# Kernel optimization log

Measured on AMD Instinct MI355X. Metric: run time of the kernel, lower is better.

The kernel has to match this reference:

```python
import math
import jax, jax.numpy as jnp
import numpy as np

NUM_PRE_NMS = 2000
NMS_THR = 0.7
MIN_SIZE = 16.0
LOG_MAX = math.log(1000.0 / 16)  # clamp on dh, dw as in the torch module

B, A, H, W = 8, 3, 200, 304
STRIDE = 4


def _make_anchors():
    # grid anchors, channel-last anchor ordering to match permute(0,2,3,1)
    sizes = np.array([32.0, 64.0, 128.0], dtype=np.float32)  # A sizes
    ys = (np.arange(H, dtype=np.float32) + 0.5) * STRIDE
    xs = (np.arange(W, dtype=np.float32) + 0.5) * STRIDE
    cy, cx = np.meshgrid(ys, xs, indexing="ij")  # [H,W]
    cx = cx[:, :, None]
    cy = cy[:, :, None]
    half = (sizes / 2.0)[None, None, :]  # [1,1,A]
    anc = np.stack([cx - half, cy - half, cx + half, cy + half], axis=-1)  # [H,W,A,4]
    anc = anc.reshape(-1, 4)  # [H*W*A, 4]
    anc = np.broadcast_to(anc[None], (B, anc.shape[0], 4)).copy()
    return jnp.asarray(anc)


def setup_inputs() -> dict:
    key = jax.random.key(0)
    k1, k2 = jax.random.split(key)
    cls_logits = jax.random.normal(k1, (B, A, H, W), dtype=jnp.float32)
    regs = jax.random.normal(k2, (B, 4 * A, H, W), dtype=jnp.float32) * 0.1
    anchors = _make_anchors()
    return {"cls_logits": cls_logits, "regs": regs, "anchors": anchors,
            "image_h": 800, "image_w": 1216}


def _box_iou(boxes):
    # boxes: [K,4] -> iou [K,K]
    x1, y1, x2, y2 = boxes[:, 0], boxes[:, 1], boxes[:, 2], boxes[:, 3]
    area = (x2 - x1) * (y2 - y1)
    ix1 = jnp.maximum(x1[:, None], x1[None, :])
    iy1 = jnp.maximum(y1[:, None], y1[None, :])
    ix2 = jnp.minimum(x2[:, None], x2[None, :])
    iy2 = jnp.minimum(y2[:, None], y2[None, :])
    iw = jnp.clip(ix2 - ix1, 0.0)
    ih = jnp.clip(iy2 - iy1, 0.0)
    inter = iw * ih
    union = area[:, None] + area[None, :] - inter
    return inter / jnp.maximum(union, 1e-6)


def _nms_one(boxes, valid):
    # boxes sorted by descending score; greedy suppression, fixed-size keep mask
    k = boxes.shape[0]
    iou = _box_iou(boxes)
    later = jnp.arange(k)

    def body(i, keep):
        sup = (iou[i] > NMS_THR) & keep[i] & (later > i)
        return keep & ~sup

    return jax.lax.fori_loop(0, k, body, valid)


def reference(cls_logits, regs, anchors, image_h, image_w):
    b = cls_logits.shape[0]
    # scores/regs in channel-last anchor order (matches permute(0,2,3,1))
    scores = jnp.transpose(cls_logits, (0, 2, 3, 1)).reshape(b, -1)       # [B,N]
    deltas = jnp.transpose(regs, (0, 2, 3, 1)).reshape(b, -1, 4)          # [B,N,4]
    n = scores.shape[1]
    k = min(NUM_PRE_NMS, n)

    top_scores, idx = jax.lax.top_k(scores, k)                            # [B,K]
    top_deltas = jnp.take_along_axis(deltas, idx[:, :, None], axis=1)     # [B,K,4]
    top_anchors = jnp.take_along_axis(anchors, idx[:, :, None], axis=1)   # [B,K,4]

    dx, dy = top_deltas[..., 0], top_deltas[..., 1]
    dh = jnp.minimum(top_deltas[..., 2], LOG_MAX)
    dw = jnp.minimum(top_deltas[..., 3], LOG_MAX)
    ah = top_anchors[..., 3] - top_anchors[..., 1]
    aw = top_anchors[..., 2] - top_anchors[..., 0]
    cx = aw / 2
    cy = ah / 2
    px = cx + dx * aw
    py = cy + dy * ah
    ph = jnp.exp(dh) * ah
    pw = jnp.exp(dw) * aw
    boxes = jnp.stack([px - pw / 2, py - ph / 2, px + pw / 2, py + ph / 2], axis=-1)  # [B,K,4]

    # size filter on clamped coords (as in _nms)
    w_img = jnp.float32(image_w)
    h_img = jnp.float32(image_h)
    bw = jnp.clip(boxes[..., 2], 0.0, w_img) - jnp.clip(boxes[..., 0], 0.0, w_img)
    bh = jnp.clip(boxes[..., 3], 0.0, h_img) - jnp.clip(boxes[..., 1], 0.0, h_img)
    valid = (bw >= MIN_SIZE) & (bh >= MIN_SIZE)

    keep = jax.vmap(_nms_one)(boxes, valid)                               # [B,K]
    out_boxes = boxes * keep[..., None].astype(boxes.dtype)
    return out_boxes, top_scores, keep
```

## Files before the change

kernel.cpp:

```cpp
#include <hip/hip_runtime.h>

#define HWSZ 60800
#define NA 3
#define NTOT 182400
#define KSEL 2000
#define CANDCAP 8192
#define NBATCH 8
#define GSPLIT 128
#define LOG_MAX_F 4.135166556742356f

#define OFF_H1    0
#define OFF_CCNT  65536
#define OFF_DONE  65568
#define ZR_BYTES  65600
#define OFF_SEL   65600
#define OFF_BOX   65728
#define OFF_VALID 321728
#define OFF_SUP   385728
#define OFF_CAND  385728
#define OFF_SUPT  4481728

__device__ __forceinline__ unsigned int xform(float f) {
    unsigned int b = __float_as_uint(f);
    return b ^ ((unsigned int)((int)b >> 31) | 0x80000000u);
}

__device__ __forceinline__ void bar_lds() {
    asm volatile("s_waitcnt lgkmcnt(0)" ::: "memory");
    __builtin_amdgcn_s_barrier();
}

__global__ __launch_bounds__(256) void k_hist_scan(const float* __restrict__ cls,
                                                   unsigned int* __restrict__ hist1,
                                                   unsigned int* __restrict__ done,
                                                   uint4* __restrict__ selinfo) {
    int b = blockIdx.y, part = blockIdx.x, tid = threadIdx.x;
    __shared__ unsigned int h[2048];
    for (int i = tid; i < 2048; i += 256) h[i] = 0u;
    __syncthreads();
    const float4* base4 = (const float4*)(cls + (size_t)b * NTOT);
    const int n4 = NTOT / 4;
    int per = (n4 + GSPLIT - 1) / GSPLIT;
    int lo = part * per, hi = lo + per;
    if (hi > n4) hi = n4;
    for (int i = lo + tid; i < hi; i += 256) {
        float4 v = base4[i];
        atomicAdd(&h[xform(v.x) >> 21], 1u);
        atomicAdd(&h[xform(v.y) >> 21], 1u);
        atomicAdd(&h[xform(v.z) >> 21], 1u);
        atomicAdd(&h[xform(v.w) >> 21], 1u);
    }
    __syncthreads();
    unsigned int* gh = hist1 + b * 2048;
    for (int i = tid; i < 2048; i += 256)
        if (h[i]) atomicAdd(&gh[i], h[i]);

    __shared__ unsigned int slast;
    __syncthreads();
    if (tid == 0) {
        __threadfence();
        unsigned int old = __hip_atomic_fetch_add(&done[b], 1u, __ATOMIC_ACQ_REL,
                                                  __HIP_MEMORY_SCOPE_AGENT);
        slast = (old == GSPLIT - 1) ? 1u : 0u;
    }
    __syncthreads();
    if (!slast) return;

    __shared__ unsigned int sa[2048], sb[2048];
    #pragma unroll
    for (int k = 0; k < 8; ++k) {
        int i = tid + k * 256;
        sa[i] = __hip_atomic_load(&gh[i], __ATOMIC_RELAXED, __HIP_MEMORY_SCOPE_AGENT);
    }
    unsigned int* src = sa; unsigned int* dst = sb;
    for (int d = 1; d < 2048; d <<= 1) {
        __syncthreads();
        #pragma unroll
        for (int k = 0; k < 8; ++k) {
            int i = tid + k * 256;
            dst[i] = src[i] + ((i + d < 2048) ? src[i + d] : 0u);
        }
        unsigned int* t = src; src = dst; dst = t;
    }
    __syncthreads();
    #pragma unroll
    for (int k = 0; k < 8; ++k) {
        int i = tid + k * 256;
        unsigned int c = src[i];
        unsigned int cn = (i < 2047) ? src[i + 1] : 0u;
        if (c >= KSEL && cn < KSEL)
            selinfo[b] = make_uint4((unsigned int)i, cn, KSEL - cn, 0u);
    }
}

__global__ __launch_bounds__(256) void k_gather(const float* __restrict__ cls,
                                                const uint4* __restrict__ selinfo,
                                                unsigned long long* __restrict__ cand,
                                                unsigned int* __restrict__ ccnt) {
    int b = blockIdx.y, part = blockIdx.x, tid = threadIdx.x;
    unsigned int bin = selinfo[b].x;
    __shared__ unsigned long long lbuf[1024];
    __shared__ unsigned int lcnt, gbase;
    if (tid == 0) lcnt = 0u;
    __syncthreads();
    const float4* base4 = (const float4*)(cls + (size_t)b * NTOT);
    const int n4 = NTOT / 4;
    int per = (n4 + GSPLIT - 1) / GSPLIT;
    int lo = part * per, hi = lo + per;
    if (hi > n4) hi = n4;
    for (int i = lo + tid; i < hi; i += 256) {
        float4 v = base4[i];
        float vals[4] = {v.x, v.y, v.z, v.w};
        int idx0 = i * 4;
        #pragma unroll
        for (int q = 0; q < 4; ++q) {
            unsigned int u = xform(vals[q]);
            if ((u >> 21) >= bin) {
                int idx = idx0 + q;
                int a = idx / HWSZ;
                int hw = idx - a * HWSZ;
                unsigned int n = (unsigned int)(hw * NA + a);
                unsigned int pos = atomicAdd(&lcnt, 1u);
                if (pos < 1024u)
                    lbuf[pos] = ((unsigned long long)u << 32) | (unsigned long long)(~n);
            }
        }
    }
    __syncthreads();
    if (tid == 0) {
        unsigned int c = lcnt < 1024u ? lcnt : 1024u;
        gbase = atomicAdd(&ccnt[b], c);
    }
    __syncthreads();
    unsigned int c = lcnt < 1024u ? lcnt : 1024u;
    unsigned int gb = gbase;
    for (unsigned int i = tid; i < c; i += 256) {
        unsigned int p = gb + i;
        if (p < CANDCAP) cand[(size_t)b * CANDCAP + p] = lbuf[i];
    }
}

__global__ __launch_bounds__(256) void k_rank_decode(
        const unsigned long long* __restrict__ cand,
        const unsigned int* __restrict__ ccnt,
        const float* __restrict__ regs,
        const float* __restrict__ anchors,
        const int* __restrict__ img_h,
        const int* __restrict__ img_w,
        float* __restrict__ out_scores,
        float4* __restrict__ boxes_ws,
        unsigned int* __restrict__ valid_ws) {
    int b = blockIdx.y;
    int tid = threadIdx.x;
    unsigned int sc = ccnt[b];
    if (sc > CANDCAP) sc = CANDCAP;
    unsigned int kbase = blockIdx.x * 64;
    if (kbase >= sc) return;
    int ki = tid & 63;
    int q = tid >> 6;
    int lane = tid & 63;
    const unsigned long long* sb_ = cand + (size_t)b * CANDCAP;
    unsigned int r = kbase + (unsigned int)ki;
    unsigned long long mykey = (r < sc) ? sb_[r] : 0ULL;

    unsigned int qs = ((sc + 255u) >> 8) << 6;
    unsigned int lo = (unsigned int)q * qs;
    unsigned int hi = lo + qs;
    if (hi > sc) hi = sc;

    unsigned int cnt = 0u;
    for (unsigned int base = lo; base < hi; base += 64) {
        unsigned long long kj = 0ULL;
        if (base + (unsigned int)lane < hi) kj = sb_[base + lane];
        unsigned int klo = (unsigned int)kj;
        unsigned int khi = (unsigned int)(kj >> 32);
        #pragma unroll
        for (int t = 0; t < 64; ++t) {
            unsigned int lo_ = (unsigned int)__builtin_amdgcn_readlane((int)klo, t);
            unsigned int hi_ = (unsigned int)__builtin_amdgcn_readlane((int)khi, t);
            unsigned long long kt = ((unsigned long long)hi_ << 32) | (unsigned long long)lo_;
            cnt += (kt > mykey) ? 1u : 0u;
        }
    }
    __shared__ unsigned int cntsh[4][64];
    cntsh[q][ki] = cnt;
    __syncthreads();
    if (tid >= 64) return;
    unsigned int rank = cntsh[0][ki] + cntsh[1][ki] + cntsh[2][ki] + cntsh[3][ki];
    if (r >= sc || rank >= KSEL) return;

    int hv = img_h[0];
    int wv = img_w[0];
    float himg = (hv > 0 && hv < 100000) ? (float)hv : __int_as_float(hv);
    float wimg = (wv > 0 && wv < 100000) ? (float)wv : __int_as_float(wv);

    unsigned int u = (unsigned int)(mykey >> 32);
    unsigned int n = ~((unsigned int)mykey);
    unsigned int bits = (u & 0x80000000u) ? (u & 0x7FFFFFFFu) : ~u;
    float score = __uint_as_float(bits);
    int a = (int)(n % NA);
    int hw = (int)(n / NA);
    const float* rp = regs + ((size_t)b * (4 * NA) + 4 * a) * HWSZ + hw;
    float dx = rp[0 * HWSZ];
    float dy = rp[1 * HWSZ];
    float dh = rp[2 * HWSZ];
    float dw = rp[3 * HWSZ];
    const float* ap = anchors + ((size_t)b * NTOT + n) * 4;
    float ax1 = ap[0], ay1 = ap[1], ax2 = ap[2], ay2 = ap[3];
    float ahh = ay2 - ay1;
    float aww = ax2 - ax1;
    float cx = aww * 0.5f;
    float cy = ahh * 0.5f;
    float px = cx + dx * aww;
    float py = cy + dy * ahh;
    dh = fminf(dh, LOG_MAX_F);
    dw = fminf(dw, LOG_MAX_F);
    float ph = expf(dh) * ahh;
    float pw = expf(dw) * aww;
    float x1 = px - pw * 0.5f;
    float y1 = py - ph * 0.5f;
    float x2 = px + pw * 0.5f;
    float y2 = py + ph * 0.5f;
    float bwv = fminf(fmaxf(x2, 0.f), wimg) - fminf(fmaxf(x1, 0.f), wimg);
    float bhv = fminf(fmaxf(y2, 0.f), himg) - fminf(fmaxf(y1, 0.f), himg);
    unsigned int valid = (bwv >= 16.f && bhv >= 16.f) ? 1u : 0u;
    size_t o = (size_t)b * KSEL + rank;
    out_scores[o] = score;
    boxes_ws[o] = make_float4(x1, y1, x2, y2);
    valid_ws[o] = valid;
}

__global__ __launch_bounds__(256) void k_supmat(const float4* __restrict__ boxes_ws,
                                                unsigned long long* __restrict__ sup,
                                                unsigned long long* __restrict__ supT) {
    int ct = blockIdx.x;
    int rt = blockIdx.y;
    int b  = blockIdx.z;
    if (ct * 64 + 63 < rt * 256) return;
    int tid = threadIdx.x;
    __shared__ float4 colbox[64];
    int j0 = ct * 64;
    if (tid < 64) {
        int jl = j0 + tid;
        colbox[tid] = (jl < KSEL) ? boxes_ws[(size_t)b * KSEL + jl]
                                  : make_float4(0.f, 0.f, 0.f, 0.f);
    }
    __syncthreads();
    int i = rt * 256 + tid;
    if (i >= KSEL) return;
    float4 bi = boxes_ws[(size_t)b * KSEL + i];
    float area_i = (bi.z - bi.x) * (bi.w - bi.y);
    unsigned long long word = 0ULL;
    #pragma unroll 8
    for (int jj = 0; jj < 64; ++jj) {
        int j = j0 + jj;
        float4 bj = colbox[jj];
        float area_j = (bj.z - bj.x) * (bj.w - bj.y);
        float ix1 = fmaxf(bi.x, bj.x);
        float iy1 = fmaxf(bi.y, bj.y);
        float ix2 = fminf(bi.z, bj.z);
        float iy2 = fminf(bi.w, bj.w);
        float iw = fmaxf(ix2 - ix1, 0.f);
        float ih = fmaxf(iy2 - iy1, 0.f);
        float inter = iw * ih;
        float uni = area_i + area_j - inter;
        float iou = inter / fmaxf(uni, 1e-6f);
        bool s = (j > i) && (j < KSEL) && (iou > 0.7f);
        if (s) word |= (1ULL << jj);
    }
    if (ct >= (i >> 6))
        sup[((size_t)b * KSEL + i) * 32 + ct] = word;

    if (ct == rt * 4 + (tid >> 6)) {
        int lane = tid & 63;
        unsigned long long cm = 0ULL;
        #pragma unroll
        for (int j = 0; j < 64; ++j) {
            unsigned long long t = __ballot((word >> j) & 1ULL);
            if (lane == j) cm = t;
        }
        supT[((size_t)b * 32 + ct) * 64 + lane] = cm;
    }
}

#define LOAD_TILE(wnext, buf)                                                \
    {                                                                        \
        int w_ = (wnext);                                                    \
        _Pragma("unroll")                                                    \
        for (int k = 0; k < 4; ++k) {                                        \
            int lr_ = (tid >> 4) + k * 16;                                   \
            int grow_ = w_ * 64 + lr_;                                       \
            if (grow_ > KSEL - 1) grow_ = KSEL - 1;                          \
            int pp_ = (2 * p + 1 >= w_) ? p : 15;                            \
            buf[k] = srowp[(size_t)grow_ * 16 + pp_];                        \
        }                                                                    \
    }

#define PROCESS_TILE(w, buf)                                                 \
    {                                                                        \
        bar_lds();                                                           \
        int w_ = (w);                                                        \
        unsigned long long pend_ =                                           \
            ((unsigned long long)accw[w_ * 2 + 1] << 32)                     \
            | (unsigned long long)accw[w_ * 2];                              \
        unsigned long long cand_ = kws[w_] & ~pend_;                         \
        unsigned int clo_ = __builtin_amdgcn_readfirstlane((unsigned int)cand_);        \
        unsigned int chi_ = __builtin_amdgcn_readfirstlane((unsigned int)(cand_ >> 32));\
        unsigned long long cur_ = ((unsigned long long)chi_ << 32)           \
                                  | (unsigned long long)clo_;                \
        if (cur_) {                                                          \
            unsigned long long cmw_ = colT[w_ * 64 + lane];                  \
            unsigned long long k_ = cur_;                                    \
            for (;;) {                                                       \
                unsigned long long sup_ = __ballot((k_ & cmw_) != 0ULL);     \
                unsigned long long k2_ = cur_ & ~sup_;                       \
                if (k2_ == k_) break;                                        \
                k_ = k2_;                                                    \
            }                                                                \
            cur_ = k_;                                                       \
            if (tid == 0) fin[w_] = cur_;                                    \
            unsigned long long v0_ = 0ULL, v1_ = 0ULL;                       \
            _Pragma("unroll")                                                \
            for (int k = 0; k < 4; ++k) {                                    \
                int lr_ = (tid >> 4) + k * 16;                               \
                if ((cur_ >> lr_) & 1ULL) { v0_ |= buf[k].x; v1_ |= buf[k].y; } \
            }                                                                \
            v0_ |= __shfl_xor(v0_, 16, 64); v0_ |= __shfl_xor(v0_, 32, 64);  \
            v1_ |= __shfl_xor(v1_, 16, 64); v1_ |= __shfl_xor(v1_, 32, 64);  \
            if (lane < 16) {                                                 \
                int wd0_ = 2 * p;                                            \
                if (wd0_ > w_ && v0_) {                                      \
                    atomicOr(&accw[wd0_ * 2], (unsigned int)v0_);            \
                    atomicOr(&accw[wd0_ * 2 + 1], (unsigned int)(v0_ >> 32));\
                }                                                            \
                if (wd0_ + 1 > w_ && v1_) {                                  \
                    atomicOr(&accw[wd0_ * 2 + 2], (unsigned int)v1_);        \
                    atomicOr(&accw[wd0_ * 2 + 3], (unsigned int)(v1_ >> 32));\
                }                                                            \
            }                                                                \
        } else if (tid == 0) {                                               \
            fin[w_] = 0ULL;                                                  \
        }                                                                    \
    }

__global__ __launch_bounds__(256) void k_nms_scan(const unsigned long long* __restrict__ sup,
                                                  const unsigned long long* __restrict__ supT,
                                                  const unsigned int* __restrict__ valid_ws,
                                                  const float4* __restrict__ boxes_ws,
                                                  float* __restrict__ out_boxes,
                                                  float* __restrict__ out_keep) {
    int b = blockIdx.x;
    int tid = threadIdx.x;
    int lane = tid & 63;
    int p = tid & 15;
    __shared__ unsigned long long kws[32];
    __shared__ unsigned long long fin[32];
    __shared__ unsigned int accw[64];
    __shared__ unsigned long long colT[32 * 64];
    const ulonglong2* srowp = (const ulonglong2*)(sup + (size_t)b * KSEL * 32);

    {
        const unsigned long long* stb = supT + (size_t)b * 2048;
        #pragma unroll
        for (int k = 0; k < 8; ++k) {
            int i = tid + k * 256;
            colT[i] = stb[i];
        }
    }

    if (tid < 32) {
        unsigned long long kw = 0ULL;
        const uint4* vv = (const uint4*)(valid_ws + (size_t)b * KSEL);
        #pragma unroll 4
        for (int q = 0; q < 16; ++q) {
            uint4 x = vv[tid * 16 + q];
            int base = q * 4;
            if (x.x) kw |= 1ULL << (base + 0);
            if (x.y) kw |= 1ULL << (base + 1);
            if (x.z) kw |= 1ULL << (base + 2);
            if (x.w) kw |= 1ULL << (base + 3);
        }
        if (tid == 31) kw &= 0xFFFFULL;
        kws[tid] = kw;
    }
    if (tid < 64) accw[tid] = 0u;

    ulonglong2 A[4], B[4], C[4], D[4];
    LOAD_TILE(0, A);
    LOAD_TILE(1, B);
    LOAD_TILE(2, C);
    LOAD_TILE(3, D);

    for (int t = 0; t < 8; ++t) {
        int w = 4 * t;
        PROCESS_TILE(w, A);
        if (w + 4 < 32) LOAD_TILE(w + 4, A);
        PROCESS_TILE(w + 1, B);
        if (w + 5 < 32) LOAD_TILE(w + 5, B);
        PROCESS_TILE(w + 2, C);
        if (w + 6 < 32) LOAD_TILE(w + 6, C);
        PROCESS_TILE(w + 3, D);
        if (w + 7 < 32) LOAD_TILE(w + 7, D);
    }
    bar_lds();

    float4* ob4 = (float4*)out_boxes;
    for (int r = tid; r < KSEL; r += 256) {
        float kf = (float)((fin[r >> 6] >> (r & 63)) & 1ULL);
        size_t o = (size_t)b * KSEL + r;
        out_keep[o] = kf;
        float4 bx = boxes_ws[o];
        ob4[o] = make_float4(bx.x * kf, bx.y * kf, bx.z * kf, bx.w * kf);
    }
}

extern "C" void kernel_launch(void* const* d_in, const int* in_sizes, int n_in,
                              void* d_out, int out_size, void* d_ws, size_t ws_size,
                              hipStream_t stream) {
    const float* cls     = (const float*)d_in[0];
    const float* regs    = (const float*)d_in[1];
    const float* anchors = (const float*)d_in[2];
    const int*   img_h   = (const int*)d_in[3];
    const int*   img_w   = (const int*)d_in[4];

    float* out = (float*)d_out;
    float* out_boxes  = out;
    float* out_scores = out + 64000;
    float* out_keep   = out + 80000;

    char* ws = (char*)d_ws;
    unsigned int* hist1      = (unsigned int*)(ws + OFF_H1);
    unsigned int* ccnt       = (unsigned int*)(ws + OFF_CCNT);
    unsigned int* done       = (unsigned int*)(ws + OFF_DONE);
    uint4* selinfo           = (uint4*)(ws + OFF_SEL);
    float4* boxes_ws         = (float4*)(ws + OFF_BOX);
    unsigned int* valid_ws   = (unsigned int*)(ws + OFF_VALID);
    unsigned long long* sup  = (unsigned long long*)(ws + OFF_SUP);
    unsigned long long* cand = (unsigned long long*)(ws + OFF_CAND);
    unsigned long long* supT = (unsigned long long*)(ws + OFF_SUPT);

    hipMemsetAsync(ws, 0, ZR_BYTES, stream);
    k_hist_scan<<<dim3(GSPLIT, NBATCH), 256, 0, stream>>>(cls, hist1, done, selinfo);
    k_gather<<<dim3(GSPLIT, NBATCH), 256, 0, stream>>>(cls, selinfo, cand, ccnt);
    k_rank_decode<<<dim3(CANDCAP / 64, NBATCH), 256, 0, stream>>>(cand, ccnt, regs, anchors,
                                                                  img_h, img_w, out_scores,
                                                                  boxes_ws, valid_ws);
    k_supmat<<<dim3(32, 8, NBATCH), 256, 0, stream>>>(boxes_ws, sup, supT);
    k_nms_scan<<<NBATCH, 256, 0, stream>>>(sup, supT, valid_ws, boxes_ws, out_boxes, out_keep);
}
```

Before: 229.5 us.

## Fuse histogram, gather and rank-decode into one persistent kernel with grid barriers

Merges the histogram/scan, candidate gather and rank/decode kernels into a single kernel of 32x8 blocks. Blocks in the same batch sync through global atomic flags and spin-waits instead of separate launches. This removes two launch boundaries and their gaps, but cuts the block count from 128 to 32 per batch, so each block streams more data and loops over rank chunks. Correctness relies on all 256 blocks being co-resident so the spin barriers cannot deadlock.

Result: slower. 257.9 us (+12.4%).

```diff
diff --git a/kernel.cpp b/kernel.cpp
--- a/kernel.cpp
+++ b/kernel.cpp
@@ -6,19 +6,21 @@
 #define KSEL 2000
 #define CANDCAP 8192
 #define NBATCH 8
-#define GSPLIT 128
+#define GSPLIT_F 32
 #define LOG_MAX_F 4.135166556742356f
 
 #define OFF_H1    0
 #define OFF_CCNT  65536
 #define OFF_DONE  65568
-#define ZR_BYTES  65600
-#define OFF_SEL   65600
-#define OFF_BOX   65728
-#define OFF_VALID 321728
-#define OFF_SUP   385728
-#define OFF_CAND  385728
-#define OFF_SUPT  4481728
+#define OFF_RDY   65600
+#define OFF_DONE2 65632
+#define ZR_BYTES  65664
+#define OFF_SEL   65664
+#define OFF_BOX   65792
+#define OFF_VALID 321792
+#define OFF_SUP   385792
+#define OFF_CAND  385792
+#define OFF_SUPT  4481792
 
 __device__ __forceinline__ unsigned int xform(float f) {
     unsigned int b = __float_as_uint(f);
@@ -30,17 +32,34 @@
     __builtin_amdgcn_s_barrier();
 }
 
-__global__ __launch_bounds__(256) void k_hist_scan(const float* __restrict__ cls,
-                                                   unsigned int* __restrict__ hist1,
-                                                   unsigned int* __restrict__ done,
-                                                   uint4* __restrict__ selinfo) {
+__global__ __launch_bounds__(256) void k_front(
+        const float* __restrict__ cls,
+        unsigned int* __restrict__ hist1,
+        unsigned int* __restrict__ done,
+        unsigned int* __restrict__ done2,
+        unsigned int* __restrict__ ready,
+        uint4* __restrict__ selinfo,
+        unsigned long long* __restrict__ cand,
+        unsigned int* __restrict__ ccnt,
+        const float* __restrict__ regs,
+        const float* __restrict__ anchors,
+        const int* __restrict__ img_h,
+        const int* __restrict__ img_w,
+        float* __restrict__ out_scores,
+        float4* __restrict__ boxes_ws,
+        unsigned int* __restrict__ valid_ws) {
     int b = blockIdx.y, part = blockIdx.x, tid = threadIdx.x;
     __shared__ unsigned int h[2048];
+    __shared__ unsigned int sa[2048], sb[2048];
+    __shared__ unsigned long long lbuf[1024];
+    __shared__ unsigned int cntsh[4][64];
+    __shared__ unsigned int lcnt, gbase, slast;
+
     for (int i = tid; i < 2048; i += 256) h[i] = 0u;
     __syncthreads();
     const float4* base4 = (const float4*)(cls + (size_t)b * NTOT);
     const int n4 = NTOT / 4;
-    int per = (n4 + GSPLIT - 1) / GSPLIT;
+    int per = (n4 + GSPLIT_F - 1) / GSPLIT_F;
     int lo = part * per, hi = lo + per;
     if (hi > n4) hi = n4;
     for (int i = lo + tid; i < hi; i += 256) {
@@ -54,60 +73,52 @@
     unsigned int* gh = hist1 + b * 2048;
     for (int i = tid; i < 2048; i += 256)
         if (h[i]) atomicAdd(&gh[i], h[i]);
-
-    __shared__ unsigned int slast;
     __syncthreads();
     if (tid == 0) {
         __threadfence();
         unsigned int old = __hip_atomic_fetch_add(&done[b], 1u, __ATOMIC_ACQ_REL,
                                                   __HIP_MEMORY_SCOPE_AGENT);
-        slast = (old == GSPLIT - 1) ? 1u : 0u;
-    }
-    __syncthreads();
-    if (!slast) return;
-
-    __shared__ unsigned int sa[2048], sb[2048];
-    #pragma unroll
-    for (int k = 0; k < 8; ++k) {
-        int i = tid + k * 256;
-        sa[i] = __hip_atomic_load(&gh[i], __ATOMIC_RELAXED, __HIP_MEMORY_SCOPE_AGENT);
-    }
-    unsigned int* src = sa; unsigned int* dst = sb;
-    for (int d = 1; d < 2048; d <<= 1) {
+        slast = (old == GSPLIT_F - 1) ? 1u : 0u;
+    }
+    __syncthreads();
+
+    if (slast) {
+        #pragma unroll
+        for (int k = 0; k < 8; ++k) {
+            int i = tid + k * 256;
+            sa[i] = __hip_atomic_load(&gh[i], __ATOMIC_RELAXED, __HIP_MEMORY_SCOPE_AGENT);
+        }
+        unsigned int* src = sa; unsigned int* dst = sb;
+        for (int d = 1; d < 2048; d <<= 1) {
+            __syncthreads();
+            #pragma unroll
+            for (int k = 0; k < 8; ++k) {
+                int i = tid + k * 256;
+                dst[i] = src[i] + ((i + d < 2048) ? src[i + d] : 0u);
+            }
+            unsigned int* t = src; src = dst; dst = t;
+        }
         __syncthreads();
         #pragma unroll
         for (int k = 0; k < 8; ++k) {
             int i = tid + k * 256;
-            dst[i] = src[i] + ((i + d < 2048) ? src[i + d] : 0u);
-        }
-        unsigned int* t = src; src = dst; dst = t;
-    }
-    __syncthreads();
-    #pragma unroll
-    for (int k = 0; k < 8; ++k) {
-        int i = tid + k * 256;
-        unsigned int c = src[i];
-        unsigned int cn = (i < 2047) ? src[i + 1] : 0u;
-        if (c >= KSEL && cn < KSEL)
-            selinfo[b] = make_uint4((unsigned int)i, cn, KSEL - cn, 0u);
-    }
-}
-
-__global__ __launch_bounds__(256) void k_gather(const float* __restrict__ cls,
-                                                const uint4* __restrict__ selinfo,
-                                                unsigned long long* __restrict__ cand,
-                                                unsigned int* __restrict__ ccnt) {
-    int b = blockIdx.y, part = blockIdx.x, tid = threadIdx.x;
+            unsigned int c = src[i];
+            unsigned int cn = (i < 2047) ? src[i + 1] : 0u;
+            if (c >= KSEL && cn < KSEL)
+                selinfo[b] = make_uint4((unsigned int)i, cn, KSEL - cn, 0u);
+        }
+        __syncthreads();
+        if (tid == 0)
+            __hip_atomic_store(&ready[b], 1u, __ATOMIC_RELEASE, __HIP_MEMORY_SCOPE_AGENT);
+    }
+
+    if (tid == 0) {
+        while (__hip_atomic_load(&ready[b], __ATOMIC_ACQUIRE, __HIP_MEMORY_SCOPE_AGENT) == 0u)
+            __builtin_amdgcn_s_sleep(2);
+        lcnt = 0u;
+    }
+    __syncthreads();
     unsigned int bin = selinfo[b].x;
-    __shared__ unsigned long long lbuf[1024];
-    __shared__ unsigned int lcnt, gbase;
-    if (tid == 0) lcnt = 0u;
-    __syncthreads();
-    const float4* base4 = (const float4*)(cls + (size_t)b * NTOT);
-    const int n4 = NTOT / 4;
-    int per = (n4 + GSPLIT - 1) / GSPLIT;
-    int lo = part * per, hi = lo + per;
-    if (hi > n4) hi = n4;
     for (int i = lo + tid; i < hi; i += 256) {
         float4 v = base4[i];
         float vals[4] = {v.x, v.y, v.z, v.w};
@@ -132,102 +143,101 @@
         gbase = atomicAdd(&ccnt[b], c);
     }
     __syncthreads();
-    unsigned int c = lcnt < 1024u ? lcnt : 1024u;
-    unsigned int gb = gbase;
-    for (unsigned int i = tid; i < c; i += 256) {
-        unsigned int p = gb + i;
-        if (p < CANDCAP) cand[(size_t)b * CANDCAP + p] = lbuf[i];
-    }
-}
-
-__global__ __launch_bounds__(256) void k_rank_decode(
-        const unsigned long long* __restrict__ cand,
-        const unsigned int* __restrict__ ccnt,
-        const float* __restrict__ regs,
-        const float* __restrict__ anchors,
-        const int* __restrict__ img_h,
-        const int* __restrict__ img_w,
-        float* __restrict__ out_scores,
-        float4* __restrict__ boxes_ws,
-        unsigned int* __restrict__ valid_ws) {
-    int b = blockIdx.y;
-    int tid = threadIdx.x;
+    {
+        unsigned int c = lcnt < 1024u ? lcnt : 1024u;
+        unsigned int gb = gbase;
+        for (unsigned int i = tid; i < c; i += 256) {
+            unsigned int p_ = gb + i;
+            if (p_ < CANDCAP) cand[(size_t)b * CANDCAP + p_] = lbuf[i];
+        }
+    }
+    __syncthreads();
+    if (tid == 0) {
+        __threadfence();
+        __hip_atomic_fetch_add(&done2[b], 1u, __ATOMIC_ACQ_REL, __HIP_MEMORY_SCOPE_AGENT);
+        while (__hip_atomic_load(&done2[b], __ATOMIC_ACQUIRE, __HIP_MEMORY_SCOPE_AGENT)
+               < (unsigned int)GSPLIT_F)
+            __builtin_amdgcn_s_sleep(2);
+    }
+    __syncthreads();
+
     unsigned int sc = ccnt[b];
     if (sc > CANDCAP) sc = CANDCAP;
-    unsigned int kbase = blockIdx.x * 64;
-    if (kbase >= sc) return;
     int ki = tid & 63;
     int q = tid >> 6;
     int lane = tid & 63;
     const unsigned long long* sb_ = cand + (size_t)b * CANDCAP;
-    unsigned int r = kbase + (unsigned int)ki;
-    unsigned long long mykey = (r < sc) ? sb_[r] : 0ULL;
-
     unsigned int qs = ((sc + 255u) >> 8) << 6;
-    unsigned int lo = (unsigned int)q * qs;
-    unsigned int hi = lo + qs;
-    if (hi > sc) hi = sc;
-
-    unsigned int cnt = 0u;
-    for (unsigned int base = lo; base < hi; base += 64) {
-        unsigned long long kj = 0ULL;
-        if (base + (unsigned int)lane < hi) kj = sb_[base + lane];
-        unsigned int klo = (unsigned int)kj;
-        unsigned int khi = (unsigned int)(kj >> 32);
-        #pragma unroll
-        for (int t = 0; t < 64; ++t) {
-            unsigned int lo_ = (unsigned int)__builtin_amdgcn_readlane((int)klo, t);
-            unsigned int hi_ = (unsigned int)__builtin_amdgcn_readlane((int)khi, t);
-            unsigned long long kt = ((unsigned long long)hi_ << 32) | (unsigned long long)lo_;
-            cnt += (kt > mykey) ? 1u : 0u;
-        }
-    }
-    __shared__ unsigned int cntsh[4][64];
-    cntsh[q][ki] = cnt;
-    __syncthreads();
-    if (tid >= 64) return;
-    unsigned int rank = cntsh[0][ki] + cntsh[1][ki] + cntsh[2][ki] + cntsh[3][ki];
-    if (r >= sc || rank >= KSEL) return;
+    unsigned int qlo = (unsigned int)q * qs;
+    unsigned int qhi = qlo + qs;
+    if (qhi > sc) qhi = sc;
 
     int hv = img_h[0];
     int wv = img_w[0];
     float himg = (hv > 0 && hv < 100000) ? (float)hv : __int_as_float(hv);
     float wimg = (wv > 0 && wv < 100000) ? (float)wv : __int_as_float(wv);
 
-    unsigned int u = (unsigned int)(mykey >> 32);
-    unsigned int n = ~((unsigned int)mykey);
-    unsigned int bits = (u & 0x80000000u) ? (u & 0x7FFFFFFFu) : ~u;
-    float score = __uint_as_float(bits);
-    int a = (int)(n % NA);
-    int hw = (int)(n / NA);
-    const float* rp = regs + ((size_t)b * (4 * NA) + 4 * a) * HWSZ + hw;
-    float dx = rp[0 * HWSZ];
-    float dy = rp[1 * HWSZ];
-    float dh = rp[2 * HWSZ];
-    float dw = rp[3 * HWSZ];
-    const float* ap = anchors + ((size_t)b * NTOT + n) * 4;
-    float ax1 = ap[0], ay1 = ap[1], ax2 = ap[2], ay2 = ap[3];
-    float ahh = ay2 - ay1;
-    float aww = ax2 - ax1;
-    float cx = aww * 0.5f;
-    float cy = ahh * 0.5f;
-    float px = cx + dx * aww;
-    float py = cy + dy * ahh;
-    dh = fminf(dh, LOG_MAX_F);
-    dw = fminf(dw, LOG_MAX_F);
-    float ph = expf(dh) * ahh;
-    float pw = expf(dw) * aww;
-    float x1 = px - pw * 0.5f;
-    float y1 = py - ph * 0.5f;
-    float x2 = px + pw * 0.5f;
-    float y2 = py + ph * 0.5f;
-    float bwv = fminf(fmaxf(x2, 0.f), wimg) - fminf(fmaxf(x1, 0.f), wimg);
-    float bhv = fminf(fmaxf(y2, 0.f), himg) - fminf(fmaxf(y1, 0.f), himg);
-    unsigned int valid = (bwv >= 16.f && bhv >= 16.f) ? 1u : 0u;
-    size_t o = (size_t)b * KSEL + rank;
-    out_scores[o] = score;
-    boxes_ws[o] = make_float4(x1, y1, x2, y2);
-    valid_ws[o] = valid;
+    for (unsigned int ch = (unsigned int)part; ch * 64u < sc; ch += GSPLIT_F) {
+        unsigned int kbase = ch * 64u;
+        unsigned int r = kbase + (unsigned int)ki;
+        unsigned long long mykey = (r < sc) ? sb_[r] : 0ULL;
+        unsigned int cnt = 0u;
+        for (unsigned int base = qlo; base < qhi; base += 64) {
+            unsigned long long kj = 0ULL;
+            if (base + (unsigned int)lane < qhi) kj = sb_[base + lane];
+            unsigned int klo = (unsigned int)kj;
+            unsigned int khi = (unsigned int)(kj >> 32);
+            #pragma unroll
+            for (int t = 0; t < 64; ++t) {
+                unsigned int lo_ = (unsigned int)__builtin_amdgcn_readlane((int)klo, t);
+                unsigned int hi_ = (unsigned int)__builtin_amdgcn_readlane((int)khi, t);
+                unsigned long long kt = ((unsigned long long)hi_ << 32) | (unsigned long long)lo_;
+                cnt += (kt > mykey) ? 1u : 0u;
+            }
+        }
+        __syncthreads();
+        cntsh[q][ki] = cnt;
+        __syncthreads();
+        if (tid < 64) {
+            unsigned int rank = cntsh[0][ki] + cntsh[1][ki] + cntsh[2][ki] + cntsh[3][ki];
+            if (r < sc && rank < KSEL) {
+                unsigned int u = (unsigned int)(mykey >> 32);
+                unsigned int n = ~((unsigned int)mykey);
+                unsigned int bits = (u & 0x80000000u) ? (u & 0x7FFFFFFFu) : ~u;
+                float score = __uint_as_float(bits);
+                int a = (int)(n % NA);
+                int hw = (int)(n / NA);
+                const float* rp = regs + ((size_t)b * (4 * NA) + 4 * a) * HWSZ + hw;
+                float dx = rp[0 * HWSZ];
+                float dy = rp[1 * HWSZ];
+                float dh = rp[2 * HWSZ];
+                float dw = rp[3 * HWSZ];
+                const float* ap = anchors + ((size_t)b * NTOT + n) * 4;
+                float ax1 = ap[0], ay1 = ap[1], ax2 = ap[2], ay2 = ap[3];
+                float ahh = ay2 - ay1;
+                float aww = ax2 - ax1;
+                float cx = aww * 0.5f;
+                float cy = ahh * 0.5f;
+                float px = cx + dx * aww;
+                float py = cy + dy * ahh;
+                dh = fminf(dh, LOG_MAX_F);
+                dw = fminf(dw, LOG_MAX_F);
+                float ph = expf(dh) * ahh;
+                float pw = expf(dw) * aww;
+                float x1 = px - pw * 0.5f;
+                float y1 = py - ph * 0.5f;
+                float x2 = px + pw * 0.5f;
+                float y2 = py + ph * 0.5f;
+                float bwv = fminf(fmaxf(x2, 0.f), wimg) - fminf(fmaxf(x1, 0.f), wimg);
+                float bhv = fminf(fmaxf(y2, 0.f), himg) - fminf(fmaxf(y1, 0.f), himg);
+                unsigned int valid = (bwv >= 16.f && bhv >= 16.f) ? 1u : 0u;
+                size_t o = (size_t)b * KSEL + rank;
+                out_scores[o] = score;
+                boxes_ws[o] = make_float4(x1, y1, x2, y2);
+                valid_ws[o] = valid;
+            }
+        }
+    }
 }
 
 __global__ __launch_bounds__(256) void k_supmat(const float4* __restrict__ boxes_ws,
@@ -432,6 +442,8 @@
     unsigned int* hist1      = (unsigned int*)(ws + OFF_H1);
     unsigned int* ccnt       = (unsigned int*)(ws + OFF_CCNT);
     unsigned int* done       = (unsigned int*)(ws + OFF_DONE);
+    unsigned int* ready      = (unsigned int*)(ws + OFF_RDY);
+    unsigned int* done2      = (unsigned int*)(ws + OFF_DONE2);
     uint4* selinfo           = (uint4*)(ws + OFF_SEL);
     float4* boxes_ws         = (float4*)(ws + OFF_BOX);
     unsigned int* valid_ws   = (unsigned int*)(ws + OFF_VALID);
@@ -440,11 +452,10 @@
     unsigned long long* supT = (unsigned long long*)(ws + OFF_SUPT);
 
     hipMemsetAsync(ws, 0, ZR_BYTES, stream);
-    k_hist_scan<<<dim3(GSPLIT, NBATCH), 256, 0, stream>>>(cls, hist1, done, selinfo);
-    k_gather<<<dim3(GSPLIT, NBATCH), 256, 0, stream>>>(cls, selinfo, cand, ccnt);
-    k_rank_decode<<<dim3(CANDCAP / 64, NBATCH), 256, 0, stream>>>(cand, ccnt, regs, anchors,
-                                                                  img_h, img_w, out_scores,
-                                                                  boxes_ws, valid_ws);
+    k_front<<<dim3(GSPLIT_F, NBATCH), 256, 0, stream>>>(cls, hist1, done, done2, ready,
+                                                        selinfo, cand, ccnt, regs, anchors,
+                                                        img_h, img_w, out_scores,
+                                                        boxes_ws, valid_ws);
     k_supmat<<<dim3(32, 8, NBATCH), 256, 0, stream>>>(boxes_ws, sup, supT);
     k_nms_scan<<<NBATCH, 256, 0, stream>>>(sup, supT, valid_ws, boxes_ws, out_boxes, out_keep);
 }
```
